# Performance work log

Measured on AMD Instinct MI355X. Metric: run time of the kernel, lower is better.

The kernel has to match this reference:

```python
import jax, jax.numpy as jnp
import numpy as np

B, N, E, K = 4, 50000, 160000, 1000
C, L = 128, 3


def setup_inputs() -> dict:
    key = jax.random.key(0)
    ks = jax.random.split(key, 16)
    x = jax.random.normal(ks[0], (B, N, 1), jnp.float32)
    edges = jax.random.randint(ks[1], (B, 2, E), 0, N)
    defense_indices = jax.random.randint(ks[2], (B, K), 0, N)
    # GIN layer MLPs: layer l is Linear(in,C) -> ReLU -> Linear(C,C); layer 0 in=1
    w1_first = jax.random.normal(ks[3], (1, C), jnp.float32) * (1.0 / np.sqrt(1))
    w1_rest = jax.random.normal(ks[4], (L - 1, C, C), jnp.float32) * (1.0 / np.sqrt(C))
    w2 = jax.random.normal(ks[5], (L, C, C), jnp.float32) * (1.0 / np.sqrt(C))
    b1 = jax.random.normal(ks[6], (L, C), jnp.float32) * 0.02
    b2 = jax.random.normal(ks[7], (L, C), jnp.float32) * 0.02
    pol_w = jax.random.normal(ks[8], (C, 1), jnp.float32) * (1.0 / np.sqrt(C))
    pol_b = jax.random.normal(ks[9], (1,), jnp.float32) * 0.02
    val_w = jax.random.normal(ks[10], (C, 1), jnp.float32) * (1.0 / np.sqrt(C))
    val_b = jax.random.normal(ks[11], (1,), jnp.float32) * 0.02
    return {"x": x, "edges": edges, "defense_indices": defense_indices,
            "nop_index": 0, "w1_first": w1_first, "w1_rest": w1_rest,
            "w2": w2, "b1": b1, "b2": b2, "pol_w": pol_w, "pol_b": pol_b,
            "val_w": val_w, "val_b": val_b}


def reference(x, edges, defense_indices, nop_index, w1_first, w1_rest, w2, b1, b2, pol_w, pol_b, val_w, val_b):
    def gin_layer(h, src, dst, w1_l, b1_l, w2_l, b2_l):
        # sum-aggregate neighbor features (source_to_target), eps = 0
        agg = jax.ops.segment_sum(h[src], dst, num_segments=N)
        z = h + agg
        return jnp.maximum(z @ w1_l + b1_l, 0.0) @ w2_l + b2_l

    def per_graph(xg, eg):
        src, dst = eg[0], eg[1]
        h = gin_layer(xg, src, dst, w1_first, b1[0], w2[0], b2[0])
        for l in range(1, L):
            h = jnp.maximum(h, 0.0)  # inter-layer activation
            h = gin_layer(h, src, dst, w1_rest[l - 1], b1[l], w2[l], b2[l])
        return h

    emb = jax.vmap(per_graph)(x, edges)       # [B, N, C]
    emb = jnp.maximum(emb, 0.0)               # self.activation after GIN
    def_emb = jax.vmap(lambda e, i: e[i])(emb, defense_indices)  # [B, K, C]
    wait = def_emb[:, nop_index, :]           # [B, C]
    policy = jnp.squeeze(def_emb @ pol_w + pol_b, -1)  # [B, K]
    value = jnp.squeeze(wait @ val_w + val_b)          # [B]
    return (policy, value)
```

## Files before the change

### kernel.cpp

```cpp
#include <hip/hip_runtime.h>
#include <hip/hip_bf16.h>

#define BB 4
#define NN 50000
#define EE 160000
#define KK 1000
#define CH 128
#define TM 64
#define NTILES ((NN + TM - 1) / TM)
#define SCAN_CHUNK 2048
#define SCAN_NB ((NN + SCAN_CHUNK - 1) / SCAN_CHUNK)

typedef unsigned short u16;
typedef unsigned int u32;
typedef __attribute__((ext_vector_type(8))) short short8;
typedef __attribute__((ext_vector_type(4))) float f32x4;

__device__ __forceinline__ int ZIDX(int m, int k) {
  return (m << 7) | (k ^ ((m & 7) << 3));
}

__device__ __forceinline__ u16 f2b(float f) {
  __hip_bfloat16 h = __float2bfloat16(f);
  return *reinterpret_cast<u16*>(&h);
}
__device__ __forceinline__ float b2f(u32 lo16) {
  return __uint_as_float(lo16 << 16);
}

__global__ __launch_bounds__(256)
void csr_count(const int* __restrict__ edges, int* __restrict__ cnt) {
  int stride = gridDim.x * blockDim.x;
  for (int i = blockIdx.x * blockDim.x + threadIdx.x; i < BB * EE; i += stride) {
    int b = i / EE, e = i - b * EE;
    int dst = edges[(b * 2 + 1) * EE + e];
    atomicAdd(&cnt[b * NN + dst], 1);
  }
}

__global__ __launch_bounds__(256)
void scan_local(const int* __restrict__ cnt, int* __restrict__ offs,
                int* __restrict__ bsum) {
  __shared__ int sdata[256];
  const int g = blockIdx.y, blk = blockIdx.x, t = threadIdx.x;
  const int i0 = blk * SCAN_CHUNK + t * 8;
  int v[8];
  int s = 0;
#pragma unroll
  for (int j = 0; j < 8; ++j) {
    int i = i0 + j;
    v[j] = (i < NN) ? cnt[g * NN + i] : 0;
    s += v[j];
  }
  sdata[t] = s;
  __syncthreads();
#pragma unroll
  for (int off = 1; off < 256; off <<= 1) {
    int vv = (t >= off) ? sdata[t - off] : 0;
    __syncthreads();
    sdata[t] += vv;
    __syncthreads();
  }
  int run = sdata[t] - s;
#pragma unroll
  for (int j = 0; j < 8; ++j) {
    int i = i0 + j;
    if (i < NN) offs[g * (NN + 1) + i] = run;
    run += v[j];
  }
  if (t == 255) bsum[g * SCAN_NB + blk] = sdata[255];
}

__global__ __launch_bounds__(256)
void scan_add(int* __restrict__ offs, int* __restrict__ woff,
              const int* __restrict__ bsum) {
  const int g = blockIdx.y, blk = blockIdx.x, t = threadIdx.x;
  int boff = 0;
  for (int j = 0; j < blk; ++j) boff += bsum[g * SCAN_NB + j];
  const int i0 = blk * SCAN_CHUNK + t * 8;
#pragma unroll
  for (int j = 0; j < 8; ++j) {
    int i = i0 + j;
    if (i < NN) {
      int val = offs[g * (NN + 1) + i] + boff;
      offs[g * (NN + 1) + i] = val;
      woff[g * NN + i] = val;
    }
  }
  if (blk == SCAN_NB - 1 && t == 255)
    offs[g * (NN + 1) + NN] = boff + bsum[g * SCAN_NB + blk];
}

__global__ __launch_bounds__(256)
void csr_fill(const int* __restrict__ edges, int* __restrict__ woff,
              int* __restrict__ csr_src) {
  int stride = gridDim.x * blockDim.x;
  for (int i = blockIdx.x * blockDim.x + threadIdx.x; i < BB * EE; i += stride) {
    int b = i / EE, e = i - b * EE;
    int src = edges[(b * 2) * EE + e];
    int dst = edges[(b * 2 + 1) * EE + e];
    int pos = atomicAdd(&woff[b * NN + dst], 1);
    csr_src[b * EE + pos] = src;
  }
}

__global__ __launch_bounds__(256)
void prep_weights(const float* __restrict__ w1r, const float* __restrict__ w2,
                  u16* __restrict__ img) {
  int i = blockIdx.x * blockDim.x + threadIdx.x;
  if (i >= 5 * CH * CH) return;
  int mat = i >> 14, rem = i & 16383;
  int k = rem >> 7, n = rem & 127;
  const float* src;
  switch (mat) {
    case 0: src = w2; break;
    case 1: src = w1r; break;
    case 2: src = w2 + 16384; break;
    case 3: src = w1r + 16384; break;
    default: src = w2 + 32768; break;
  }
  img[(mat << 14) + ZIDX(n, k)] = f2b(src[(k << 7) + n]);
}

template <bool L0>
__global__ __launch_bounds__(256)
void gin_layer(const void* __restrict__ hin_v, u16* __restrict__ hout,
               const int* __restrict__ offs, const int* __restrict__ csr_src,
               const float* __restrict__ w1f,
               const u16* __restrict__ img_w1,
               const u16* __restrict__ img_w2,
               const float* __restrict__ b1v, const float* __restrict__ b2v) {
  __shared__ u16 zt[TM * CH];
  __shared__ u16 wt[CH * CH];
  __shared__ float part[L0 ? TM * 4 : 1];

  const int tid = threadIdx.x;
  const int lane = tid & 63;
  const int wv = tid >> 6;
  const int g = lane >> 4;
  const int lr = lane & 15;
  const int cb = wv * 32;

  const int tile = blockIdx.x;
  const int b = tile / NTILES;
  const int t0 = (tile - b * NTILES) * TM;
  const int nm = min(TM, NN - t0);

  {
    const uint4* src = (const uint4*)(L0 ? img_w2 : img_w1);
    uint4* dst = (uint4*)wt;
    for (int i = tid; i < 2048; i += 256) dst[i] = src[i];
  }

  const int m = tid >> 2;
  const int p = tid & 3;
  const int gnode = t0 + m;
  int start = 0, end = 0;
  if (m < nm) {
    start = offs[b * (NN + 1) + gnode];
    end = offs[b * (NN + 1) + gnode + 1];
  }

  if (L0) {
    const float* x = (const float*)hin_v;
    float s = 0.f;
    if (m < nm) {
      if (p == 0) s = x[b * NN + gnode];
      for (int e = start + p; e < end; e += 4) s += x[b * NN + csr_src[b * EE + e]];
    }
    part[(m << 2) + p] = s;
    __syncthreads();
    float z0 = part[m << 2] + part[(m << 2) + 1] + part[(m << 2) + 2] +
               part[(m << 2) + 3];
    for (int j = 0; j < 4; ++j) {
      int c0 = (p << 5) + (j << 3);
      short8 tv;
#pragma unroll
      for (int t = 0; t < 8; ++t)
        tv[t] = (short)f2b(fmaxf(z0 * w1f[c0 + t] + b1v[c0 + t], 0.f));
      *(short8*)&zt[ZIDX(m, c0)] = tv;
    }
    __syncthreads();
  } else {
    const u16* h = (const u16*)hin_v;
    float acc[32];
#pragma unroll
    for (int t = 0; t < 32; ++t) acc[t] = 0.f;
    if (m < nm) {
      {
        const uint4* hr = (const uint4*)(h + ((size_t)(b * NN + gnode) << 7));
#pragma unroll
        for (int j = 0; j < 4; ++j) {
          uint4 v = hr[(p << 2) + j];
          acc[j*8+0] += b2f(v.x & 0xffff); acc[j*8+1] += b2f(v.x >> 16);
          acc[j*8+2] += b2f(v.y & 0xffff); acc[j*8+3] += b2f(v.y >> 16);
          acc[j*8+4] += b2f(v.z & 0xffff); acc[j*8+5] += b2f(v.z >> 16);
          acc[j*8+6] += b2f(v.w & 0xffff); acc[j*8+7] += b2f(v.w >> 16);
        }
      }
      for (int e = start; e < end; ++e) {
        int src = csr_src[b * EE + e];
        const uint4* hr = (const uint4*)(h + ((size_t)(b * NN + src) << 7));
#pragma unroll
        for (int j = 0; j < 4; ++j) {
          uint4 v = hr[(p << 2) + j];
          acc[j*8+0] += b2f(v.x & 0xffff); acc[j*8+1] += b2f(v.x >> 16);
          acc[j*8+2] += b2f(v.y & 0xffff); acc[j*8+3] += b2f(v.y >> 16);
          acc[j*8+4] += b2f(v.z & 0xffff); acc[j*8+5] += b2f(v.z >> 16);
          acc[j*8+6] += b2f(v.w & 0xffff); acc[j*8+7] += b2f(v.w >> 16);
        }
      }
    }
    for (int j = 0; j < 4; ++j) {
      int c0 = (p << 5) + (j << 3);
      short8 tv;
#pragma unroll
      for (int t = 0; t < 8; ++t) tv[t] = (short)f2b(acc[(j << 3) + t]);
      *(short8*)&zt[ZIDX(m, c0)] = tv;
    }
    __syncthreads();

    f32x4 a1[4][2];
#pragma unroll
    for (int rt = 0; rt < 4; ++rt)
#pragma unroll
      for (int ct = 0; ct < 2; ++ct) a1[rt][ct] = (f32x4){0.f, 0.f, 0.f, 0.f};
#pragma unroll
    for (int k0 = 0; k0 < CH; k0 += 32) {
      int kb = k0 + (g << 3);
      short8 af[4], bfr[2];
#pragma unroll
      for (int rt = 0; rt < 4; ++rt)
        af[rt] = *(const short8*)&zt[ZIDX((rt << 4) + lr, kb)];
#pragma unroll
      for (int ct = 0; ct < 2; ++ct)
        bfr[ct] = *(const short8*)&wt[ZIDX(cb + (ct << 4) + lr, kb)];
#pragma unroll
      for (int rt = 0; rt < 4; ++rt)
#pragma unroll
        for (int ct = 0; ct < 2; ++ct)
          a1[rt][ct] = __builtin_amdgcn_mfma_f32_16x16x32_bf16(
              af[rt], bfr[ct], a1[rt][ct], 0, 0, 0);
    }
    __syncthreads();

    {
      const uint4* src = (const uint4*)img_w2;
      uint4* dst = (uint4*)wt;
      for (int i = tid; i < 2048; i += 256) dst[i] = src[i];
    }
#pragma unroll
    for (int rt = 0; rt < 4; ++rt)
#pragma unroll
      for (int ct = 0; ct < 2; ++ct) {
        int col = cb + (ct << 4) + lr;
        float bias = b1v[col];
#pragma unroll
        for (int r = 0; r < 4; ++r) {
          int row = (rt << 4) + (g << 2) + r;
          zt[ZIDX(row, col)] = f2b(fmaxf(a1[rt][ct][r] + bias, 0.f));
        }
      }
    __syncthreads();
  }

  f32x4 a2[4][2];
#pragma unroll
  for (int rt = 0; rt < 4; ++rt)
#pragma unroll
    for (int ct = 0; ct < 2; ++ct) a2[rt][ct] = (f32x4){0.f, 0.f, 0.f, 0.f};
#pragma unroll
  for (int k0 = 0; k0 < CH; k0 += 32) {
    int kb = k0 + (g << 3);
    short8 af[4], bfr[2];
#pragma unroll
    for (int rt = 0; rt < 4; ++rt)
      af[rt] = *(const short8*)&zt[ZIDX((rt << 4) + lr, kb)];
#pragma unroll
    for (int ct = 0; ct < 2; ++ct)
      bfr[ct] = *(const short8*)&wt[ZIDX(cb + (ct << 4) + lr, kb)];
#pragma unroll
    for (int rt = 0; rt < 4; ++rt)
#pragma unroll
      for (int ct = 0; ct < 2; ++ct)
        a2[rt][ct] = __builtin_amdgcn_mfma_f32_16x16x32_bf16(
            af[rt], bfr[ct], a2[rt][ct], 0, 0, 0);
  }
  __syncthreads();

#pragma unroll
  for (int rt = 0; rt < 4; ++rt)
#pragma unroll
    for (int ct = 0; ct < 2; ++ct) {
      int col = cb + (ct << 4) + lr;
      float bias = b2v[col];
#pragma unroll
      for (int r = 0; r < 4; ++r) {
        int row = (rt << 4) + (g << 2) + r;
        zt[ZIDX(row, col)] = f2b(fmaxf(a2[rt][ct][r] + bias, 0.f));
      }
    }
  __syncthreads();

  for (int i = tid; i < 1024; i += 256) {
    int mm = i >> 4, c0 = (i & 15) << 3;
    if (mm < nm) {
      uint4 v = *(const uint4*)&zt[ZIDX(mm, c0)];
      *(uint4*)&hout[(((size_t)(b * NN + t0 + mm)) << 7) + c0] = v;
    }
  }
}

__global__ __launch_bounds__(256)
void heads_kernel(const u16* __restrict__ emb, const int* __restrict__ didx,
                  const int* __restrict__ nopp, const float* __restrict__ pol_w,
                  const float* __restrict__ pol_b, const float* __restrict__ val_w,
                  const float* __restrict__ val_b, float* __restrict__ out) {
  int gw = (blockIdx.x * blockDim.x + threadIdx.x) >> 6;
  int lane = threadIdx.x & 63;
  if (gw >= BB * KK) return;
  int b = gw / KK, k = gw - b * KK;
  int node = didx[b * KK + k];
  const u16* e = emb + (((size_t)(b * NN + node)) << 7);
  u32 v = *(const u32*)&e[lane << 1];
  float f0 = __uint_as_float(v << 16);
  float f1 = __uint_as_float(v & 0xffff0000u);
  float s = f0 * pol_w[lane << 1] + f1 * pol_w[(lane << 1) + 1];
#pragma unroll
  for (int off = 32; off; off >>= 1) s += __shfl_down(s, off);
  if (lane == 0) out[b * KK + k] = s + pol_b[0];
  if (k == nopp[0]) {
    float vv = f0 * val_w[lane << 1] + f1 * val_w[(lane << 1) + 1];
#pragma unroll
    for (int off = 32; off; off >>= 1) vv += __shfl_down(vv, off);
    if (lane == 0) out[BB * KK + b] = vv + val_b[0];
  }
}

extern "C" void kernel_launch(void* const* d_in, const int* in_sizes, int n_in,
                              void* d_out, int out_size, void* d_ws, size_t ws_size,
                              hipStream_t stream) {
  const float* x     = (const float*)d_in[0];
  const int*   edges = (const int*)d_in[1];
  const int*   didx  = (const int*)d_in[2];
  const int*   nopp  = (const int*)d_in[3];
  const float* w1f   = (const float*)d_in[4];
  const float* w1r   = (const float*)d_in[5];
  const float* w2    = (const float*)d_in[6];
  const float* b1    = (const float*)d_in[7];
  const float* b2    = (const float*)d_in[8];
  const float* pol_w = (const float*)d_in[9];
  const float* pol_b = (const float*)d_in[10];
  const float* val_w = (const float*)d_in[11];
  const float* val_b = (const float*)d_in[12];
  float* out = (float*)d_out;

  char* ws = (char*)d_ws;
  u16* hA = (u16*)ws;            ws += (size_t)BB * NN * CH * 2;
  u16* hB = (u16*)ws;            ws += (size_t)BB * NN * CH * 2;
  u16* img = (u16*)ws;           ws += (size_t)5 * CH * CH * 2;
  int* offs = (int*)ws;          ws += (size_t)BB * (NN + 1) * 4;
  int* woff = (int*)ws;          ws += (size_t)BB * NN * 4;
  int* cnt  = (int*)ws;          ws += (size_t)BB * NN * 4;
  int* bsum = (int*)ws;          ws += (size_t)BB * SCAN_NB * 4;
  int* csr  = (int*)ws;          ws += (size_t)BB * EE * 4;

  hipMemsetAsync(cnt, 0, (size_t)BB * NN * 4, stream);
  prep_weights<<<(5 * CH * CH + 255) / 256, 256, 0, stream>>>(w1r, w2, img);
  csr_count<<<1250, 256, 0, stream>>>(edges, cnt);
  scan_local<<<dim3(SCAN_NB, BB), 256, 0, stream>>>(cnt, offs, bsum);
  scan_add<<<dim3(SCAN_NB, BB), 256, 0, stream>>>(offs, woff, bsum);
  csr_fill<<<1250, 256, 0, stream>>>(edges, woff, csr);

  const int tiles = BB * NTILES;
  gin_layer<true><<<tiles, 256, 0, stream>>>(
      x, hA, offs, csr, w1f, nullptr, img, b1, b2);
  gin_layer<false><<<tiles, 256, 0, stream>>>(
      hA, hB, offs, csr, nullptr, img + 1 * 16384, img + 2 * 16384,
      b1 + CH, b2 + CH);
  gin_layer<false><<<tiles, 256, 0, stream>>>(
      hB, hA, offs, csr, nullptr, img + 3 * 16384, img + 4 * 16384,
      b1 + 2 * CH, b2 + 2 * CH);

  heads_kernel<<<(BB * KK * 64 + 255) / 256, 256, 0, stream>>>(
      hA, didx, nopp, pol_w, pol_b, val_w, val_b, out);
}
```

Baseline: 331.8 us.

## Edge-balanced LDS atomic aggregation and register-resident weight fragments in GIN layers

Replaces per-node serial neighbor loops with a tile-wide edge range split evenly across waves. Each wave accumulates into an fp32 LDS buffer using a stored local destination index and LDS atomics, which removes load imbalance from skewed degrees. Weight matrices are no longer copied into LDS; each wave loads its MFMA B fragments straight from global memory into registers, using a plain row-major image. This lowers LDS use and adds a launch-bounds occupancy hint. The cost is eight LDS float atomics per 16 bytes of gathered data, plus a new byte array written during CSR construction.

```diff
diff --git a/kernel.cpp b/kernel.cpp
--- a/kernel.cpp
+++ b/kernel.cpp
@@ -10,9 +10,11 @@
 #define NTILES ((NN + TM - 1) / TM)
 #define SCAN_CHUNK 2048
 #define SCAN_NB ((NN + SCAN_CHUNK - 1) / SCAN_CHUNK)
+#define FPAD 132
 
 typedef unsigned short u16;
 typedef unsigned int u32;
+typedef unsigned char u8;
 typedef __attribute__((ext_vector_type(8))) short short8;
 typedef __attribute__((ext_vector_type(4))) float f32x4;
 
@@ -93,7 +95,7 @@
 
 __global__ __launch_bounds__(256)
 void csr_fill(const int* __restrict__ edges, int* __restrict__ woff,
-              int* __restrict__ csr_src) {
+              int* __restrict__ csr_src, u8* __restrict__ csr_dst) {
   int stride = gridDim.x * blockDim.x;
   for (int i = blockIdx.x * blockDim.x + threadIdx.x; i < BB * EE; i += stride) {
     int b = i / EE, e = i - b * EE;
@@ -101,6 +103,7 @@
     int dst = edges[(b * 2 + 1) * EE + e];
     int pos = atomicAdd(&woff[b * NN + dst], 1);
     csr_src[b * EE + pos] = src;
+    csr_dst[b * EE + pos] = (u8)(dst & 63);
   }
 }
 
@@ -119,20 +122,22 @@
     case 3: src = w1r + 16384; break;
     default: src = w2 + 32768; break;
   }
-  img[(mat << 14) + ZIDX(n, k)] = f2b(src[(k << 7) + n]);
+  img[(mat << 14) + (n << 7) + k] = f2b(src[(k << 7) + n]);
 }
 
 template <bool L0>
-__global__ __launch_bounds__(256)
+__global__ __launch_bounds__(256, 4)
 void gin_layer(const void* __restrict__ hin_v, u16* __restrict__ hout,
                const int* __restrict__ offs, const int* __restrict__ csr_src,
+               const u8* __restrict__ csr_dst,
                const float* __restrict__ w1f,
                const u16* __restrict__ img_w1,
                const u16* __restrict__ img_w2,
                const float* __restrict__ b1v, const float* __restrict__ b2v) {
-  __shared__ u16 zt[TM * CH];
-  __shared__ u16 wt[CH * CH];
-  __shared__ float part[L0 ? TM * 4 : 1];
+  __shared__ float zaccf[TM * FPAD];
+  __shared__ float zacc0[L0 ? TM : 1];
+  u16* zt = (u16*)zaccf;
+  u16* ot = (u16*)zaccf + 8192;
 
   const int tid = threadIdx.x;
   const int lane = tid & 63;
@@ -141,114 +146,147 @@
   const int lr = lane & 15;
   const int cb = wv * 32;
 
-  const int tile = blockIdx.x;
-  const int b = tile / NTILES;
-  const int t0 = (tile - b * NTILES) * TM;
+  const int b = blockIdx.x / NTILES;
+  const int t0 = (blockIdx.x % NTILES) * TM;
   const int nm = min(TM, NN - t0);
 
-  {
-    const uint4* src = (const uint4*)(L0 ? img_w2 : img_w1);
-    uint4* dst = (uint4*)wt;
-    for (int i = tid; i < 2048; i += 256) dst[i] = src[i];
-  }
+  const int s0 = offs[b * (NN + 1) + t0];
+  const int e0 = offs[b * (NN + 1) + min(t0 + TM, NN)];
 
   const int m = tid >> 2;
   const int p = tid & 3;
-  const int gnode = t0 + m;
-  int start = 0, end = 0;
-  if (m < nm) {
-    start = offs[b * (NN + 1) + gnode];
-    end = offs[b * (NN + 1) + gnode + 1];
-  }
+
+  short8 fw2[2][4];
+#pragma unroll
+  for (int ct = 0; ct < 2; ++ct)
+#pragma unroll
+    for (int ks = 0; ks < 4; ++ks)
+      fw2[ct][ks] = *(const short8*)&img_w2[((cb + (ct << 4) + lr) << 7) +
+                                            (ks << 5) + (g << 3)];
 
   if (L0) {
     const float* x = (const float*)hin_v;
-    float s = 0.f;
-    if (m < nm) {
-      if (p == 0) s = x[b * NN + gnode];
-      for (int e = start + p; e < end; e += 4) s += x[b * NN + csr_src[b * EE + e]];
-    }
-    part[(m << 2) + p] = s;
-    __syncthreads();
-    float z0 = part[m << 2] + part[(m << 2) + 1] + part[(m << 2) + 2] +
-               part[(m << 2) + 3];
-    for (int j = 0; j < 4; ++j) {
-      int c0 = (p << 5) + (j << 3);
-      short8 tv;
-#pragma unroll
-      for (int t = 0; t < 8; ++t)
-        tv[t] = (short)f2b(fmaxf(z0 * w1f[c0 + t] + b1v[c0 + t], 0.f));
-      *(short8*)&zt[ZIDX(m, c0)] = tv;
+    if (tid < TM) zacc0[tid] = (tid < nm) ? x[b * NN + t0 + tid] : 0.f;
+    __syncthreads();
+    {
+      int M = e0 - s0;
+      int Mw = (M + 3) >> 2;
+      int wstart = s0 + wv * Mw;
+      int wend = min(wstart + Mw, e0);
+      for (int e = wstart + lane; e < wend; e += 64) {
+        int src = csr_src[b * EE + e];
+        int dstl = csr_dst[b * EE + e];
+        unsafeAtomicAdd(&zacc0[dstl], x[b * NN + src]);
+      }
+    }
+    __syncthreads();
+    {
+      float z0 = zacc0[m];
+#pragma unroll
+      for (int jj = 0; jj < 4; ++jj) {
+        int c0 = (p << 5) + (jj << 3);
+        short8 tv;
+#pragma unroll
+        for (int t = 0; t < 8; ++t)
+          tv[t] = (short)f2b(fmaxf(z0 * w1f[c0 + t] + b1v[c0 + t], 0.f));
+        *(short8*)&zt[ZIDX(m, c0)] = tv;
+      }
     }
     __syncthreads();
   } else {
     const u16* h = (const u16*)hin_v;
-    float acc[32];
-#pragma unroll
-    for (int t = 0; t < 32; ++t) acc[t] = 0.f;
     if (m < nm) {
-      {
-        const uint4* hr = (const uint4*)(h + ((size_t)(b * NN + gnode) << 7));
-#pragma unroll
-        for (int j = 0; j < 4; ++j) {
-          uint4 v = hr[(p << 2) + j];
-          acc[j*8+0] += b2f(v.x & 0xffff); acc[j*8+1] += b2f(v.x >> 16);
-          acc[j*8+2] += b2f(v.y & 0xffff); acc[j*8+3] += b2f(v.y >> 16);
-          acc[j*8+4] += b2f(v.z & 0xffff); acc[j*8+5] += b2f(v.z >> 16);
-          acc[j*8+6] += b2f(v.w & 0xffff); acc[j*8+7] += b2f(v.w >> 16);
+      const uint4* hr =
+          (const uint4*)(h + ((size_t)(b * NN + t0 + m) << 7)) + (p << 2);
+      float* zr = &zaccf[m * FPAD + (p << 5)];
+#pragma unroll
+      for (int j = 0; j < 4; ++j) {
+        uint4 v = hr[j];
+        zr[j * 8 + 0] = b2f(v.x & 0xffff); zr[j * 8 + 1] = b2f(v.x >> 16);
+        zr[j * 8 + 2] = b2f(v.y & 0xffff); zr[j * 8 + 3] = b2f(v.y >> 16);
+        zr[j * 8 + 4] = b2f(v.z & 0xffff); zr[j * 8 + 5] = b2f(v.z >> 16);
+        zr[j * 8 + 6] = b2f(v.w & 0xffff); zr[j * 8 + 7] = b2f(v.w >> 16);
+      }
+    } else {
+      float* zr = &zaccf[m * FPAD + (p << 5)];
+#pragma unroll
+      for (int j = 0; j < 32; ++j) zr[j] = 0.f;
+    }
+    __syncthreads();
+
+    {
+      int M = e0 - s0;
+      int Mw = (M + 3) >> 2;
+      int wstart = s0 + wv * Mw;
+      int wend = min(wstart + Mw, e0);
+      int Mww = wend - wstart;
+      if (Mww > 0) {
+        int R = (Mww + 15) >> 4;
+        int g4 = lane >> 2;
+        for (int r = 0; r < R; ++r) {
+          int ei = g4 * R + r;
+          if (ei < Mww) {
+            int e = wstart + ei;
+            int src = csr_src[b * EE + e];
+            int dstl = csr_dst[b * EE + e];
+            const uint4* hr =
+                (const uint4*)(h + ((size_t)(b * NN + src) << 7)) + (p << 2);
+            float* zr = &zaccf[dstl * FPAD + (p << 5)];
+#pragma unroll
+            for (int j = 0; j < 4; ++j) {
+              uint4 v = hr[j];
+              unsafeAtomicAdd(&zr[j * 8 + 0], b2f(v.x & 0xffff));
+              unsafeAtomicAdd(&zr[j * 8 + 1], b2f(v.x >> 16));
+              unsafeAtomicAdd(&zr[j * 8 + 2], b2f(v.y & 0xffff));
+              unsafeAtomicAdd(&zr[j * 8 + 3], b2f(v.y >> 16));
+              unsafeAtomicAdd(&zr[j * 8 + 4], b2f(v.z & 0xffff));
+              unsafeAtomicAdd(&zr[j * 8 + 5], b2f(v.z >> 16));
+              unsafeAtomicAdd(&zr[j * 8 + 6], b2f(v.w & 0xffff));
+              unsafeAtomicAdd(&zr[j * 8 + 7], b2f(v.w >> 16));
+            }
+          }
         }
       }
-      for (int e = start; e < end; ++e) {
-        int src = csr_src[b * EE + e];
-        const uint4* hr = (const uint4*)(h + ((size_t)(b * NN + src) << 7));
-#pragma unroll
-        for (int j = 0; j < 4; ++j) {
-          uint4 v = hr[(p << 2) + j];
-          acc[j*8+0] += b2f(v.x & 0xffff); acc[j*8+1] += b2f(v.x >> 16);
-          acc[j*8+2] += b2f(v.y & 0xffff); acc[j*8+3] += b2f(v.y >> 16);
-          acc[j*8+4] += b2f(v.z & 0xffff); acc[j*8+5] += b2f(v.z >> 16);
-          acc[j*8+6] += b2f(v.w & 0xffff); acc[j*8+7] += b2f(v.w >> 16);
-        }
-      }
-    }
-    for (int j = 0; j < 4; ++j) {
-      int c0 = (p << 5) + (j << 3);
-      short8 tv;
-#pragma unroll
-      for (int t = 0; t < 8; ++t) tv[t] = (short)f2b(acc[(j << 3) + t]);
-      *(short8*)&zt[ZIDX(m, c0)] = tv;
-    }
-    __syncthreads();
-
+    }
+    __syncthreads();
+
+    short8 fw1[2][4];
+#pragma unroll
+    for (int ct = 0; ct < 2; ++ct)
+#pragma unroll
+      for (int ks = 0; ks < 4; ++ks)
+        fw1[ct][ks] = *(const short8*)&img_w1[((cb + (ct << 4) + lr) << 7) +
+                                              (ks << 5) + (g << 3)];
     f32x4 a1[4][2];
 #pragma unroll
     for (int rt = 0; rt < 4; ++rt)
 #pragma unroll
       for (int ct = 0; ct < 2; ++ct) a1[rt][ct] = (f32x4){0.f, 0.f, 0.f, 0.f};
 #pragma unroll
-    for (int k0 = 0; k0 < CH; k0 += 32) {
-      int kb = k0 + (g << 3);
-      short8 af[4], bfr[2];
-#pragma unroll
-      for (int rt = 0; rt < 4; ++rt)
-        af[rt] = *(const short8*)&zt[ZIDX((rt << 4) + lr, kb)];
-#pragma unroll
-      for (int ct = 0; ct < 2; ++ct)
-        bfr[ct] = *(const short8*)&wt[ZIDX(cb + (ct << 4) + lr, kb)];
+    for (int ks = 0; ks < 4; ++ks) {
+      int kb = (ks << 5) + (g << 3);
+      short8 af[4];
+#pragma unroll
+      for (int rt = 0; rt < 4; ++rt) {
+        const float* zr = &zaccf[((rt << 4) + lr) * FPAD + kb];
+        f32x4 lo = *(const f32x4*)zr;
+        f32x4 hi = *(const f32x4*)(zr + 4);
+        short8 a;
+        a[0] = (short)f2b(lo[0]); a[1] = (short)f2b(lo[1]);
+        a[2] = (short)f2b(lo[2]); a[3] = (short)f2b(lo[3]);
+        a[4] = (short)f2b(hi[0]); a[5] = (short)f2b(hi[1]);
+        a[6] = (short)f2b(hi[2]); a[7] = (short)f2b(hi[3]);
+        af[rt] = a;
+      }
 #pragma unroll
       for (int rt = 0; rt < 4; ++rt)
 #pragma unroll
         for (int ct = 0; ct < 2; ++ct)
           a1[rt][ct] = __builtin_amdgcn_mfma_f32_16x16x32_bf16(
-              af[rt], bfr[ct], a1[rt][ct], 0, 0, 0);
-    }
-    __syncthreads();
-
-    {
-      const uint4* src = (const uint4*)img_w2;
-      uint4* dst = (uint4*)wt;
-      for (int i = tid; i < 2048; i += 256) dst[i] = src[i];
-    }
+              af[rt], fw1[ct][ks], a1[rt][ct], 0, 0, 0);
+    }
+    __syncthreads();
+
 #pragma unroll
     for (int rt = 0; rt < 4; ++rt)
 #pragma unroll
@@ -270,23 +308,19 @@
 #pragma unroll
     for (int ct = 0; ct < 2; ++ct) a2[rt][ct] = (f32x4){0.f, 0.f, 0.f, 0.f};
 #pragma unroll
-  for (int k0 = 0; k0 < CH; k0 += 32) {
-    int kb = k0 + (g << 3);
-    short8 af[4], bfr[2];
+  for (int ks = 0; ks < 4; ++ks) {
+    int kb = (ks << 5) + (g << 3);
+    short8 af[4];
 #pragma unroll
     for (int rt = 0; rt < 4; ++rt)
       af[rt] = *(const short8*)&zt[ZIDX((rt << 4) + lr, kb)];
 #pragma unroll
-    for (int ct = 0; ct < 2; ++ct)
-      bfr[ct] = *(const short8*)&wt[ZIDX(cb + (ct << 4) + lr, kb)];
-#pragma unroll
     for (int rt = 0; rt < 4; ++rt)
 #pragma unroll
       for (int ct = 0; ct < 2; ++ct)
         a2[rt][ct] = __builtin_amdgcn_mfma_f32_16x16x32_bf16(
-            af[rt], bfr[ct], a2[rt][ct], 0, 0, 0);
-  }
-  __syncthreads();
+            af[rt], fw2[ct][ks], a2[rt][ct], 0, 0, 0);
+  }
 
 #pragma unroll
   for (int rt = 0; rt < 4; ++rt)
@@ -297,7 +331,7 @@
 #pragma unroll
       for (int r = 0; r < 4; ++r) {
         int row = (rt << 4) + (g << 2) + r;
-        zt[ZIDX(row, col)] = f2b(fmaxf(a2[rt][ct][r] + bias, 0.f));
+        ot[ZIDX(row, col)] = f2b(fmaxf(a2[rt][ct][r] + bias, 0.f));
       }
     }
   __syncthreads();
@@ -305,7 +339,7 @@
   for (int i = tid; i < 1024; i += 256) {
     int mm = i >> 4, c0 = (i & 15) << 3;
     if (mm < nm) {
-      uint4 v = *(const uint4*)&zt[ZIDX(mm, c0)];
+      uint4 v = *(const uint4*)&ot[ZIDX(mm, c0)];
       *(uint4*)&hout[(((size_t)(b * NN + t0 + mm)) << 7) + c0] = v;
     }
   }
@@ -364,22 +398,23 @@
   int* cnt  = (int*)ws;          ws += (size_t)BB * NN * 4;
   int* bsum = (int*)ws;          ws += (size_t)BB * SCAN_NB * 4;
   int* csr  = (int*)ws;          ws += (size_t)BB * EE * 4;
+  u8*  csrd = (u8*)ws;           ws += (size_t)BB * EE;
 
   hipMemsetAsync(cnt, 0, (size_t)BB * NN * 4, stream);
   prep_weights<<<(5 * CH * CH + 255) / 256, 256, 0, stream>>>(w1r, w2, img);
   csr_count<<<1250, 256, 0, stream>>>(edges, cnt);
   scan_local<<<dim3(SCAN_NB, BB), 256, 0, stream>>>(cnt, offs, bsum);
   scan_add<<<dim3(SCAN_NB, BB), 256, 0, stream>>>(offs, woff, bsum);
-  csr_fill<<<1250, 256, 0, stream>>>(edges, woff, csr);
+  csr_fill<<<1250, 256, 0, stream>>>(edges, woff, csr, csrd);
 
   const int tiles = BB * NTILES;
   gin_layer<true><<<tiles, 256, 0, stream>>>(
-      x, hA, offs, csr, w1f, nullptr, img, b1, b2);
+      x, hA, offs, csr, csrd, w1f, nullptr, img, b1, b2);
   gin_layer<false><<<tiles, 256, 0, stream>>>(
-      hA, hB, offs, csr, nullptr, img + 1 * 16384, img + 2 * 16384,
+      hA, hB, offs, csr, csrd, nullptr, img + 1 * 16384, img + 2 * 16384,
       b1 + CH, b2 + CH);
   gin_layer<false><<<tiles, 256, 0, stream>>>(
-      hB, hA, offs, csr, nullptr, img + 3 * 16384, img + 4 * 16384,
+      hB, hA, offs, csr, csrd, nullptr, img + 3 * 16384, img + 4 * 16384,
       b1 + 2 * CH, b2 + 2 * CH);
 
   heads_kernel<<<(BB * KK * 64 + 255) / 256, 256, 0, stream>>>(
```

After: 1.123 ms. 3.38x slower.
